# Optimization experiments

Measured on AMD Instinct MI355X. Metric: run time of the kernel, lower is better.

Reference implementation:

```python
import jax, jax.numpy as jnp
import numpy as np

B, H, W, D = 2, 32, 32, 32
C = 384          # hidden_dim
HEADS = 6
HD = C // HEADS  # head dim = 64
NNOISE = 256
EPS = 1e-5


def setup_inputs() -> dict:
    key = jax.random.key(0)
    ks = jax.random.split(key, 8)
    rnd = lambda k, shape, sc=0.02: jax.random.normal(k, shape, jnp.float32) * sc
    return {
        "x": rnd(ks[0], (B, H, W, D, C), 1.0),
        "x_noise": rnd(ks[1], (B, NNOISE), 1.0),
        # AdaLN generator: Linear(NNOISE, 6*C) after SiLU (zero_init=False -> random)
        "ada_w": rnd(ks[2], (NNOISE, 6 * C)),
        "ada_b": jnp.zeros((6 * C,), jnp.float32),
        # fused qkv projection Linear(C, 3C)
        "qkv_w": rnd(ks[3], (C, 3 * C)),
        "qkv_b": jnp.zeros((3 * C,), jnp.float32),
        # output projection Linear(C, C)
        "out_w": rnd(ks[4], (C, C)),
        "out_b": jnp.zeros((C,), jnp.float32),
        # MLP: Linear(C,4C) -> GELU -> Linear(4C,C)
        "mlp_w1": rnd(ks[5], (C, 4 * C)),
        "mlp_b1": jnp.zeros((4 * C,), jnp.float32),
        "mlp_w2": rnd(ks[6], (4 * C, C)),
        "mlp_b2": jnp.zeros((C,), jnp.float32),
    }


def _layernorm(x):
    # LayerNorm over last dim, no affine (use_ada_ln=True)
    mu = jnp.mean(x, axis=-1, keepdims=True)
    var = jnp.mean(jnp.square(x - mu), axis=-1, keepdims=True)
    return (x - mu) * jax.lax.rsqrt(var + EPS)


def _mod(x, shift, scale):
    # modulate: x*(1+scale)+shift, broadcast [B,C] over spatial dims
    return x * (1.0 + scale[:, None, None, None, :]) + shift[:, None, None, None, :]


def _gate(x, g):
    return x * g[:, None, None, None, :]


def _axial_attn(q, k, v, axis):
    # q,k,v: [B,H,W,D,heads,hd]; attend along spatial `axis` (1, 2 or 3)
    q1 = jnp.moveaxis(q, axis, -2)  # [..., heads, S, hd]
    k1 = jnp.moveaxis(k, axis, -2)
    v1 = jnp.moveaxis(v, axis, -2)
    scores = jnp.einsum('...sc,...tc->...st', q1, k1) * (1.0 / np.sqrt(HD))
    attn = jax.nn.softmax(scores, axis=-1)
    o = jnp.einsum('...st,...tc->...sc', attn, v1)
    return jnp.moveaxis(o, -2, axis)


def reference(x, x_noise, ada_w, ada_b, qkv_w, qkv_b, out_w, out_b,
              mlp_w1, mlp_b1, mlp_w2, mlp_b2):
    # AdaLN params from noise embedding
    params = jax.nn.silu(x_noise) @ ada_w + ada_b  # [B, 6C]
    shift1, scale1, gate1, shift2, scale2, gate2 = jnp.split(params, 6, axis=-1)

    norm_x = _mod(_layernorm(x), shift1, scale1)
    qkv = norm_x @ qkv_w + qkv_b                  # [B,H,W,D,3C]
    q, k, v = jnp.split(qkv, 3, axis=-1)
    split_heads = lambda t: t.reshape(*t.shape[:-1], HEADS, HD)
    q, k, v = split_heads(q), split_heads(k), split_heads(v)

    # three axial attentions (over D, W, H), summed
    out = _axial_attn(q, k, v, 3) + _axial_attn(q, k, v, 2) + _axial_attn(q, k, v, 1)
    out = out.reshape(B, H, W, D, C)
    out = _gate(out @ out_w + out_b, gate1)
    x = x + out

    h = _mod(_layernorm(x), shift2, scale2)
    h = jax.nn.gelu(h @ mlp_w1 + mlp_b1, approximate=False) @ mlp_w2 + mlp_b2
    return x + _gate(h, gate2)
```

## Files before the change

### kernel.cpp

```cpp
#include <hip/hip_runtime.h>
#include <hip/hip_bf16.h>
#include <math.h>

#define TOKENS 65536
#define C_DIM 384
#define SIXC 2304
#define SEQ 32

typedef __attribute__((ext_vector_type(8))) short short8;
typedef __attribute__((ext_vector_type(4))) float f32x4;

__device__ __forceinline__ float bf2f(unsigned short u) {
    return __uint_as_float(((unsigned int)u) << 16);
}
__device__ __forceinline__ unsigned short f2bf(float f) {
    unsigned int u = __float_as_uint(f);
    u += 0x7fffu + ((u >> 16) & 1u);
    return (unsigned short)(u >> 16);
}

__global__ __launch_bounds__(256) void ada_kernel(
    const float* __restrict__ xn, const float* __restrict__ aw,
    const float* __restrict__ ab, float* __restrict__ params)
{
    __shared__ float sx[256];
    int b = blockIdx.y;
    int n = blockIdx.x * 256 + threadIdx.x;
    float xv = xn[b * 256 + threadIdx.x];
    sx[threadIdx.x] = xv / (1.0f + __expf(-xv));
    __syncthreads();
    float acc = ab[n];
    for (int k = 0; k < 256; ++k)
        acc += sx[k] * aw[(size_t)k * SIXC + n];
    params[b * SIXC + n] = acc;
}

__global__ __launch_bounds__(256) void transpose_w_kernel(
    const float* __restrict__ W, unsigned short* __restrict__ WT, int K, int N)
{
    __shared__ float t[32][33];
    int kb = blockIdx.x * 32, nb = blockIdx.y * 32;
    int tn = threadIdx.x & 31, t8 = threadIdx.x >> 5;
#pragma unroll
    for (int i = 0; i < 4; ++i) {
        int k = t8 + i * 8;
        t[k][tn] = W[(size_t)(kb + k) * N + nb + tn];
    }
    __syncthreads();
#pragma unroll
    for (int i = 0; i < 4; ++i) {
        int n = t8 + i * 8;
        WT[(size_t)(nb + n) * K + kb + tn] = f2bf(t[tn][n]);
    }
}

template<int IN_F32>
__global__ __launch_bounds__(256) void ln_mod_kernel(
    const void* __restrict__ inp, unsigned short* __restrict__ out,
    const float* __restrict__ params, int shift_off, int scale_off)
{
    int t = blockIdx.x * 4 + (threadIdx.x >> 6);
    int lane = threadIdx.x & 63;
    float v[6];
    float s = 0.f, s2 = 0.f;
    if (IN_F32) {
        const float* px = (const float*)inp + (size_t)t * C_DIM;
#pragma unroll
        for (int j = 0; j < 6; ++j) { v[j] = px[lane + (j << 6)]; s += v[j]; s2 += v[j] * v[j]; }
    } else {
        const unsigned short* px = (const unsigned short*)inp + (size_t)t * C_DIM;
#pragma unroll
        for (int j = 0; j < 6; ++j) { v[j] = bf2f(px[lane + (j << 6)]); s += v[j]; s2 += v[j] * v[j]; }
    }
#pragma unroll
    for (int m = 32; m >= 1; m >>= 1) {
        s += __shfl_xor(s, m, 64);
        s2 += __shfl_xor(s2, m, 64);
    }
    float mean = s * (1.0f / 384.0f);
    float var = s2 * (1.0f / 384.0f) - mean * mean;
    float rs = rsqrtf(var + 1e-5f);
    int b = t >> 15;
    const float* shp = params + b * SIXC + shift_off;
    const float* scp = params + b * SIXC + scale_off;
    unsigned short* po = out + (size_t)t * C_DIM;
#pragma unroll
    for (int j = 0; j < 6; ++j) {
        int c = lane + (j << 6);
        po[c] = f2bf((v[j] - mean) * rs * (1.0f + scp[c]) + shp[c]);
    }
}

template<int EPI, int RESF32, int OUTF32>
__global__ __launch_bounds__(512) void gemm_kernel(
    const unsigned short* __restrict__ Ab,
    const unsigned short* __restrict__ WT, const float* __restrict__ bias,
    void* __restrict__ outp, int M, int N, int K,
    const void* __restrict__ res, const float* __restrict__ params,
    int gate_off)
{
    __shared__ __align__(16) unsigned short As[128][40];
    __shared__ __align__(16) unsigned short Bs[384][40];
    int tid = threadIdx.x;
    int lane = tid & 63;
    int wave = tid >> 6;
    int wm = wave >> 2;
    int wn = wave & 3;
    int bn0 = blockIdx.x * 384;
    int bm0 = blockIdx.y * 128;

    f32x4 acc[4][6] = {};

    int arow = tid >> 2, akc = (tid & 3) << 3;
    int nk = K >> 5;
    for (int kt = 0; kt < nk; ++kt) {
        {
            size_t gofs = (size_t)(bm0 + arow) * K + (kt << 5) + akc;
            *(uint4*)&As[arow][akc] = *(const uint4*)(Ab + gofs);
        }
#pragma unroll
        for (int cc = 0; cc < 3; ++cc) {
            int idx = tid + cc * 512;
            int row = idx >> 2, kc = (idx & 3) << 3;
            size_t gofs = (size_t)(bn0 + row) * K + (kt << 5) + kc;
            *(uint4*)&Bs[row][kc] = *(const uint4*)(WT + gofs);
        }
        __syncthreads();
        int kg = (lane >> 4) << 3;
        int lr = lane & 15;
        short8 af[4], bf[6];
#pragma unroll
        for (int mi = 0; mi < 4; ++mi)
            af[mi] = *(const short8*)&As[wm * 64 + mi * 16 + lr][kg];
#pragma unroll
        for (int ni = 0; ni < 6; ++ni)
            bf[ni] = *(const short8*)&Bs[wn * 96 + ni * 16 + lr][kg];
#pragma unroll
        for (int ni = 0; ni < 6; ++ni)
#pragma unroll
            for (int mi = 0; mi < 4; ++mi)
                acc[mi][ni] = __builtin_amdgcn_mfma_f32_16x16x32_bf16(af[mi], bf[ni], acc[mi][ni], 0, 0, 0);
        __syncthreads();
    }

    int lc = lane & 15;
    int lrow = (lane >> 4) << 2;
#pragma unroll
    for (int mi = 0; mi < 4; ++mi) {
#pragma unroll
        for (int ni = 0; ni < 6; ++ni) {
            int col = bn0 + wn * 96 + ni * 16 + lc;
            float bv = bias[col];
#pragma unroll
            for (int r = 0; r < 4; ++r) {
                int row = bm0 + wm * 64 + mi * 16 + lrow + r;
                float v = acc[mi][ni][r] + bv;
                size_t oofs = (size_t)row * N + col;
                if (EPI == 1) {
                    v = 0.5f * v * (1.0f + erff(v * 0.70710678118f));
                } else if (EPI == 2) {
                    int b = row >> 15;
                    float rv = RESF32 ? ((const float*)res)[oofs]
                                      : bf2f(((const unsigned short*)res)[oofs]);
                    v = rv + params[b * SIXC + gate_off + col] * v;
                }
                if (OUTF32) ((float*)outp)[oofs] = v;
                else        ((unsigned short*)outp)[oofs] = f2bf(v);
            }
        }
    }
}

__global__ __launch_bounds__(256) void attn_kernel(
    const unsigned short* __restrict__ qkv, unsigned short* __restrict__ attn_out,
    int stride, int first)
{
    __shared__ float qs[32][66], ks[32][66], vs[32][66];
    __shared__ float ss[32][33];
    int g = blockIdx.x, head = blockIdx.y;
    int o = g / stride, i0 = g - o * stride;
    int base = o * (SEQ * stride) + i0;
    int tid = threadIdx.x;
    int row = tid >> 3, gq = tid & 7;
    int tok = base + row * stride;
    size_t qbase = (size_t)tok * 1152 + head * 64 + gq * 8;
    {
        uint4 vq = *(const uint4*)(qkv + qbase);
        uint4 vk = *(const uint4*)(qkv + qbase + 384);
        uint4 vv = *(const uint4*)(qkv + qbase + 768);
        const unsigned short* pq = (const unsigned short*)&vq;
        const unsigned short* pk = (const unsigned short*)&vk;
        const unsigned short* pv = (const unsigned short*)&vv;
#pragma unroll
        for (int j = 0; j < 8; ++j) {
            qs[row][gq * 8 + j] = bf2f(pq[j]);
            ks[row][gq * 8 + j] = bf2f(pk[j]);
            vs[row][gq * 8 + j] = bf2f(pv[j]);
        }
    }
    __syncthreads();

    float sj[4];
#pragma unroll
    for (int jj = 0; jj < 4; ++jj) {
        int j = gq + jj * 8;
        float s = 0.f;
        for (int c = 0; c < 64; ++c) s += qs[row][c] * ks[j][c];
        sj[jj] = s * 0.125f;
    }
    float mx = fmaxf(fmaxf(sj[0], sj[1]), fmaxf(sj[2], sj[3]));
#pragma unroll
    for (int m = 1; m < 8; m <<= 1) mx = fmaxf(mx, __shfl_xor(mx, m, 8));
    float sum = 0.f;
#pragma unroll
    for (int jj = 0; jj < 4; ++jj) {
        float e = __expf(sj[jj] - mx);
        ss[row][gq + jj * 8] = e;
        sum += e;
    }
#pragma unroll
    for (int m = 1; m < 8; m <<= 1) sum += __shfl_xor(sum, m, 8);
    float inv = 1.0f / sum;
    __syncthreads();

    float ov[8] = {0.f, 0.f, 0.f, 0.f, 0.f, 0.f, 0.f, 0.f};
    for (int j = 0; j < 32; ++j) {
        float p = ss[row][j];
#pragma unroll
        for (int c8 = 0; c8 < 8; ++c8) ov[c8] += p * vs[j][gq * 8 + c8];
    }
    unsigned short* dst = attn_out + (size_t)tok * C_DIM + head * 64 + gq * 8;
    if (first) {
#pragma unroll
        for (int c8 = 0; c8 < 8; ++c8) dst[c8] = f2bf(ov[c8] * inv);
    } else {
#pragma unroll
        for (int c8 = 0; c8 < 8; ++c8) dst[c8] = f2bf(bf2f(dst[c8]) + ov[c8] * inv);
    }
}

extern "C" void kernel_launch(void* const* d_in, const int* in_sizes, int n_in,
                              void* d_out, int out_size, void* d_ws, size_t ws_size,
                              hipStream_t stream) {
    const float* x      = (const float*)d_in[0];
    const float* xnoise = (const float*)d_in[1];
    const float* ada_w  = (const float*)d_in[2];
    const float* ada_b  = (const float*)d_in[3];
    const float* qkv_w  = (const float*)d_in[4];
    const float* qkv_b  = (const float*)d_in[5];
    const float* out_w  = (const float*)d_in[6];
    const float* out_b  = (const float*)d_in[7];
    const float* mlp_w1 = (const float*)d_in[8];
    const float* mlp_b1 = (const float*)d_in[9];
    const float* mlp_w2 = (const float*)d_in[10];
    const float* mlp_b2 = (const float*)d_in[11];

    char* ws = (char*)d_ws;
    float* params = (float*)ws;
    unsigned short* wt_qkv = (unsigned short*)(ws + 32768);
    unsigned short* wt_out = wt_qkv + 442368;
    unsigned short* wt_m1  = wt_out + 147456;
    unsigned short* wt_m2  = wt_m1 + 589824;
    unsigned short* Areg = (unsigned short*)(ws + 32768 + 4194304UL);
    unsigned short* Breg = Areg + 25165824UL;

    ada_kernel<<<dim3(9, 2), 256, 0, stream>>>(xnoise, ada_w, ada_b, params);
    transpose_w_kernel<<<dim3(12, 36), 256, 0, stream>>>(qkv_w, wt_qkv, 384, 1152);
    transpose_w_kernel<<<dim3(12, 12), 256, 0, stream>>>(out_w, wt_out, 384, 384);
    transpose_w_kernel<<<dim3(12, 48), 256, 0, stream>>>(mlp_w1, wt_m1, 384, 1536);
    transpose_w_kernel<<<dim3(48, 12), 256, 0, stream>>>(mlp_w2, wt_m2, 1536, 384);

    ln_mod_kernel<1><<<16384, 256, 0, stream>>>(x, Areg, params, 0, 384);
    gemm_kernel<0, 0, 0><<<dim3(3, 512), 512, 0, stream>>>(Areg, wt_qkv, qkv_b, Breg,
                                                           TOKENS, 1152, 384, nullptr, nullptr, 0);
    attn_kernel<<<dim3(2048, 6), 256, 0, stream>>>(Breg, Areg, 1, 1);
    attn_kernel<<<dim3(2048, 6), 256, 0, stream>>>(Breg, Areg, 32, 0);
    attn_kernel<<<dim3(2048, 6), 256, 0, stream>>>(Breg, Areg, 1024, 0);
    gemm_kernel<2, 1, 1><<<dim3(1, 512), 512, 0, stream>>>(Areg, wt_out, out_b, d_out,
                                                           TOKENS, 384, 384, x, params, 768);
    ln_mod_kernel<1><<<16384, 256, 0, stream>>>(d_out, Areg, params, 1152, 1536);
    gemm_kernel<1, 0, 0><<<dim3(4, 512), 512, 0, stream>>>(Areg, wt_m1, mlp_b1, Breg,
                                                           TOKENS, 1536, 384, nullptr, nullptr, 0);
    gemm_kernel<2, 1, 1><<<dim3(1, 512), 512, 0, stream>>>(Breg, wt_m2, mlp_b2, d_out,
                                                           TOKENS, 384, 1536, d_out, params, 1920);
}
```

Baseline: 1.145 ms.

## Use direct global-to-LDS loads, head-major QKV layout, bf16 residual intermediates

The GEMM now stages A and B tiles with global_load_lds straight into unpadded LDS, skipping the round trip through registers. The QKV GEMM gets a new epilogue that writes Q, K and V in a head-major [3*heads][tokens][64] layout, so the attention kernels read contiguous 128-byte rows per token instead of strided 2304-byte rows. The post-attention residual is kept in bf16 in scratch rather than fp32 in the output buffer, which cuts intermediate traffic. The costs are possible LDS bank conflicts from dropping the padding and some precision loss in the residual stream.

Measured after the change: 1.166 ms. About the same (+1.9%).

```diff
diff --git a/kernel.cpp b/kernel.cpp
--- a/kernel.cpp
+++ b/kernel.cpp
@@ -9,6 +9,8 @@
 
 typedef __attribute__((ext_vector_type(8))) short short8;
 typedef __attribute__((ext_vector_type(4))) float f32x4;
+typedef __attribute__((address_space(3))) unsigned char lds_byte;
+typedef __attribute__((address_space(1))) const unsigned char glb_byte;
 
 __device__ __forceinline__ float bf2f(unsigned short u) {
     return __uint_as_float(((unsigned int)u) << 16);
@@ -99,8 +101,8 @@
     const void* __restrict__ res, const float* __restrict__ params,
     int gate_off)
 {
-    __shared__ __align__(16) unsigned short As[128][40];
-    __shared__ __align__(16) unsigned short Bs[384][40];
+    __shared__ __align__(16) unsigned short As[128 * 32];
+    __shared__ __align__(16) unsigned short Bs[384 * 32];
     int tid = threadIdx.x;
     int lane = tid & 63;
     int wave = tid >> 6;
@@ -111,19 +113,20 @@
 
     f32x4 acc[4][6] = {};
 
-    int arow = tid >> 2, akc = (tid & 3) << 3;
+    int srow = lane >> 2;
+    int skc = (lane & 3) << 3;
     int nk = K >> 5;
     for (int kt = 0; kt < nk; ++kt) {
+        int k0 = kt << 5;
         {
-            size_t gofs = (size_t)(bm0 + arow) * K + (kt << 5) + akc;
-            *(uint4*)&As[arow][akc] = *(const uint4*)(Ab + gofs);
-        }
-#pragma unroll
-        for (int cc = 0; cc < 3; ++cc) {
-            int idx = tid + cc * 512;
-            int row = idx >> 2, kc = (idx & 3) << 3;
-            size_t gofs = (size_t)(bn0 + row) * K + (kt << 5) + kc;
-            *(uint4*)&Bs[row][kc] = *(const uint4*)(WT + gofs);
+            const unsigned short* gp = Ab + (size_t)(bm0 + wave * 16 + srow) * K + k0 + skc;
+            __builtin_amdgcn_global_load_lds((glb_byte*)gp, (lds_byte*)&As[wave * 16 * 32], 16, 0, 0);
+        }
+#pragma unroll
+        for (int j = 0; j < 3; ++j) {
+            int r0 = (wave * 3 + j) << 4;
+            const unsigned short* gp = WT + (size_t)(bn0 + r0 + srow) * K + k0 + skc;
+            __builtin_amdgcn_global_load_lds((glb_byte*)gp, (lds_byte*)&Bs[r0 * 32], 16, 0, 0);
         }
         __syncthreads();
         int kg = (lane >> 4) << 3;
@@ -131,10 +134,10 @@
         short8 af[4], bf[6];
 #pragma unroll
         for (int mi = 0; mi < 4; ++mi)
-            af[mi] = *(const short8*)&As[wm * 64 + mi * 16 + lr][kg];
+            af[mi] = *(const short8*)&As[(wm * 64 + mi * 16 + lr) * 32 + kg];
 #pragma unroll
         for (int ni = 0; ni < 6; ++ni)
-            bf[ni] = *(const short8*)&Bs[wn * 96 + ni * 16 + lr][kg];
+            bf[ni] = *(const short8*)&Bs[(wn * 96 + ni * 16 + lr) * 32 + kg];
 #pragma unroll
         for (int ni = 0; ni < 6; ++ni)
 #pragma unroll
@@ -155,17 +158,26 @@
             for (int r = 0; r < 4; ++r) {
                 int row = bm0 + wm * 64 + mi * 16 + lrow + r;
                 float v = acc[mi][ni][r] + bv;
-                size_t oofs = (size_t)row * N + col;
                 if (EPI == 1) {
                     v = 0.5f * v * (1.0f + erff(v * 0.70710678118f));
                 } else if (EPI == 2) {
+                    size_t oofs = (size_t)row * N + col;
                     int b = row >> 15;
                     float rv = RESF32 ? ((const float*)res)[oofs]
                                       : bf2f(((const unsigned short*)res)[oofs]);
                     v = rv + params[b * SIXC + gate_off + col] * v;
                 }
-                if (OUTF32) ((float*)outp)[oofs] = v;
-                else        ((unsigned short*)outp)[oofs] = f2bf(v);
+                if (EPI == 3) {
+                    int p = col / 384;
+                    int head = (col - p * 384) >> 6;
+                    int hd = col & 63;
+                    size_t oofs = ((size_t)(p * 6 + head) << 22) + ((size_t)row << 6) + hd;
+                    ((unsigned short*)outp)[oofs] = f2bf(v);
+                } else {
+                    size_t oofs = (size_t)row * N + col;
+                    if (OUTF32) ((float*)outp)[oofs] = v;
+                    else        ((unsigned short*)outp)[oofs] = f2bf(v);
+                }
             }
         }
     }
@@ -183,11 +195,11 @@
     int tid = threadIdx.x;
     int row = tid >> 3, gq = tid & 7;
     int tok = base + row * stride;
-    size_t qbase = (size_t)tok * 1152 + head * 64 + gq * 8;
+    size_t tofs = ((size_t)tok << 6) + gq * 8;
     {
-        uint4 vq = *(const uint4*)(qkv + qbase);
-        uint4 vk = *(const uint4*)(qkv + qbase + 384);
-        uint4 vv = *(const uint4*)(qkv + qbase + 768);
+        uint4 vq = *(const uint4*)(qkv + (((size_t)head) << 22) + tofs);
+        uint4 vk = *(const uint4*)(qkv + (((size_t)(6 + head)) << 22) + tofs);
+        uint4 vv = *(const uint4*)(qkv + (((size_t)(12 + head)) << 22) + tofs);
         const unsigned short* pq = (const unsigned short*)&vq;
         const unsigned short* pk = (const unsigned short*)&vk;
         const unsigned short* pv = (const unsigned short*)&vv;
@@ -263,6 +275,7 @@
     unsigned short* wt_m2  = wt_m1 + 589824;
     unsigned short* Areg = (unsigned short*)(ws + 32768 + 4194304UL);
     unsigned short* Breg = Areg + 25165824UL;
+    unsigned short* hin  = (unsigned short*)d_out;
 
     ada_kernel<<<dim3(9, 2), 256, 0, stream>>>(xnoise, ada_w, ada_b, params);
     transpose_w_kernel<<<dim3(12, 36), 256, 0, stream>>>(qkv_w, wt_qkv, 384, 1152);
@@ -271,16 +284,16 @@
     transpose_w_kernel<<<dim3(48, 12), 256, 0, stream>>>(mlp_w2, wt_m2, 1536, 384);
 
     ln_mod_kernel<1><<<16384, 256, 0, stream>>>(x, Areg, params, 0, 384);
-    gemm_kernel<0, 0, 0><<<dim3(3, 512), 512, 0, stream>>>(Areg, wt_qkv, qkv_b, Breg,
+    gemm_kernel<3, 0, 0><<<dim3(3, 512), 512, 0, stream>>>(Areg, wt_qkv, qkv_b, Breg,
                                                            TOKENS, 1152, 384, nullptr, nullptr, 0);
     attn_kernel<<<dim3(2048, 6), 256, 0, stream>>>(Breg, Areg, 1, 1);
     attn_kernel<<<dim3(2048, 6), 256, 0, stream>>>(Breg, Areg, 32, 0);
     attn_kernel<<<dim3(2048, 6), 256, 0, stream>>>(Breg, Areg, 1024, 0);
-    gemm_kernel<2, 1, 1><<<dim3(1, 512), 512, 0, stream>>>(Areg, wt_out, out_b, d_out,
+    gemm_kernel<2, 1, 0><<<dim3(1, 512), 512, 0, stream>>>(Areg, wt_out, out_b, Areg,
                                                            TOKENS, 384, 384, x, params, 768);
-    ln_mod_kernel<1><<<16384, 256, 0, stream>>>(d_out, Areg, params, 1152, 1536);
-    gemm_kernel<1, 0, 0><<<dim3(4, 512), 512, 0, stream>>>(Areg, wt_m1, mlp_b1, Breg,
+    ln_mod_kernel<0><<<16384, 256, 0, stream>>>(Areg, hin, params, 1152, 1536);
+    gemm_kernel<1, 0, 0><<<dim3(4, 512), 512, 0, stream>>>(hin, wt_m1, mlp_b1, Breg,
                                                            TOKENS, 1536, 384, nullptr, nullptr, 0);
-    gemm_kernel<2, 1, 1><<<dim3(1, 512), 512, 0, stream>>>(Breg, wt_m2, mlp_b2, d_out,
-                                                           TOKENS, 384, 1536, d_out, params, 1920);
-}
+    gemm_kernel<2, 0, 1><<<dim3(1, 512), 512, 0, stream>>>(Breg, wt_m2, mlp_b2, d_out,
+                                                           TOKENS, 384, 1536, Areg, params, 1920);
+}
```
